# Performance work log

Hardware: AMD Instinct MI355X
Metric: run time of the kernel (lower is better)

The kernel has to match this reference:

```python
import jax, jax.numpy as jnp
import numpy as np

N = 400000
C = 256
H = 512
B = 1024


def setup_inputs() -> dict:
    key = jax.random.key(0)
    k1, k2, k3, k4, k5, k6 = jax.random.split(key, 6)
    x = jax.random.normal(k1, (N, C), dtype=jnp.float32)
    batch = jnp.sort(jax.random.randint(k2, (N,), 0, B, dtype=jnp.int64))
    # Linear params (torch nn.Linear layout: W [out, in], y = x @ W.T + b)
    Wt = jax.random.normal(k3, (H, C), dtype=jnp.float32) / np.sqrt(C)
    bt = jax.random.normal(k4, (H,), dtype=jnp.float32) * 0.01
    Wg = jax.random.normal(k5, (1, H), dtype=jnp.float32) / np.sqrt(H)
    bg = jax.random.normal(k6, (1,), dtype=jnp.float32) * 0.01
    return {"x": x, "batch": batch, "batch_size": B,
            "Wt": Wt, "bt": bt, "Wg": Wg, "bg": bg}


def reference(x, batch, batch_size, Wt, bt, Wg, bg):
    # gate: softplus(Linear(x)) -> Linear -> scalar attention logit per node
    nx = jax.nn.softplus(x @ Wt.T + bt)          # [N, 512]
    logits = (nx @ Wg.T + bg)[:, 0]              # [N]
    # scatter softmax over segments (numerically stable)
    seg_max = jax.ops.segment_max(logits, batch, num_segments=batch_size)
    e = jnp.exp(logits - seg_max[batch])         # [N]
    seg_sum = jax.ops.segment_sum(e, batch, num_segments=batch_size)
    attn = (e / seg_sum[batch])[:, None]         # [N, 1]
    # weighted sum + segment mean
    out_sum = jax.ops.segment_sum(attn * x, batch, num_segments=batch_size)  # [B, C]
    x_sum = jax.ops.segment_sum(x, batch, num_segments=batch_size)
    counts = jax.ops.segment_sum(jnp.ones((x.shape[0],), x.dtype), batch,
                                 num_segments=batch_size)
    mean = x_sum / jnp.maximum(counts, 1.0)[:, None]
    return out_sum + mean
```

## Files before the change

kernel.cpp:

```cpp
#include <hip/hip_runtime.h>
#include <hip/hip_bf16.h>
#include <stdint.h>

typedef __attribute__((ext_vector_type(8))) short short8;
typedef __attribute__((ext_vector_type(16))) float f32x16;

#define CD 256
#define HD 512

static __device__ __forceinline__ unsigned short f2bf(float f) {
    union { float f; unsigned int u; } cv; cv.f = f;
    unsigned int u = cv.u;
    unsigned int r = u + 0x7FFFu + ((u >> 16) & 1u);
    return (unsigned short)(r >> 16);
}
static __device__ __forceinline__ unsigned int pack2(unsigned short a, unsigned short b) {
    return (unsigned int)a | ((unsigned int)b << 16);
}

__global__ void prep_kernel(const float* __restrict__ wt, unsigned short* __restrict__ wtb,
                            const void* __restrict__ batch, int* __restrict__ b32, int n) {
    const int blk = blockIdx.x;
    if (blk < 64) {
        int t = blk * 256 + threadIdx.x;
        const float4* p = (const float4*)wt;
        float4 f0 = p[t * 2], f1 = p[t * 2 + 1];
        uint4 v;
        v.x = pack2(f2bf(f0.x), f2bf(f0.y));
        v.y = pack2(f2bf(f0.z), f2bf(f0.w));
        v.z = pack2(f2bf(f1.x), f2bf(f1.y));
        v.w = pack2(f2bf(f1.z), f2bf(f1.w));
        ((uint4*)wtb)[t] = v;
    } else {
        const long long* p64 = (const long long*)batch;
        const int* p32 = (const int*)batch;
        bool is64 = ((unsigned long long)p64[n / 2 - 1]) < (1ull << 20);
        for (int i = (blk - 64) * 256 + threadIdx.x; i < n; i += 512 * 256)
            b32[i] = is64 ? (int)p64[i] : p32[i];
    }
}

__global__ __launch_bounds__(256) void gate_kernel(
    const float* __restrict__ x, const unsigned short* __restrict__ wtb,
    const float* __restrict__ bt, const float* __restrict__ wg,
    const float* __restrict__ bg, float* __restrict__ logits, int n)
{
    __shared__ __align__(16) char lds[36864];
    const int tid = threadIdx.x;
    const int lane = tid & 63;
    const int wid = tid >> 6;
    const int l31 = lane & 31;
    const int g = lane >> 5;
    const long rowbase = (long)blockIdx.x * 128;

    {
        float2 b2 = ((const float2*)bt)[tid];
        float2 w2 = ((const float2*)wg)[tid];
        *(float2*)(lds + 32768 + tid * 8) = b2;
        *(float2*)(lds + 34816 + tid * 8) = w2;
    }

    short8 a[16];
    {
        const long row = rowbase + wid * 32 + l31;
        const float4* xr = (const float4*)(x + row * 256) + g * 2;
#define CVT_A(kt, F0, F1)                                                             \
        {                                                                             \
            __hip_bfloat162 p0 = __float22bfloat162_rn(make_float2((F0).x, (F0).y));  \
            __hip_bfloat162 p1 = __float22bfloat162_rn(make_float2((F0).z, (F0).w));  \
            __hip_bfloat162 p2 = __float22bfloat162_rn(make_float2((F1).x, (F1).y));  \
            __hip_bfloat162 p3 = __float22bfloat162_rn(make_float2((F1).z, (F1).w));  \
            union { uint4 u; short8 s; } cv;                                          \
            cv.u = make_uint4(*(unsigned int*)&p0, *(unsigned int*)&p1,               \
                              *(unsigned int*)&p2, *(unsigned int*)&p3);              \
            a[kt] = cv.s;                                                             \
        }
        if (rowbase + 128 <= (long)n) {
#pragma unroll
            for (int kt = 0; kt < 16; ++kt) {
                float4 f0 = xr[kt * 4];
                float4 f1 = xr[kt * 4 + 1];
                CVT_A(kt, f0, f1)
            }
        } else {
            const bool ok = row < (long)n;
#pragma unroll
            for (int kt = 0; kt < 16; ++kt) {
                float4 f0 = ok ? xr[kt * 4]     : make_float4(0.f, 0.f, 0.f, 0.f);
                float4 f1 = ok ? xr[kt * 4 + 1] : make_float4(0.f, 0.f, 0.f, 0.f);
                CVT_A(kt, f0, f1)
            }
        }
#undef CVT_A
    }

    int soff[4];
#pragma unroll
    for (int i = 0; i < 4; ++i) {
        int p = (wid * 4 + i) * 64 + lane;
        int rc = p >> 5;
        int gcl = (p & 31) ^ (rc & 31);
        soff[i] = rc * 512 + gcl * 16;
    }
    const char* wtbb = (const char*)wtb;

#define STAGE(c, bufoff)                                                              \
    {                                                                                 \
        const char* src = wtbb + (c) * 16384;                                         \
        char* dst = lds + (bufoff) + wid * 4096;                                      \
        _Pragma("unroll")                                                             \
        for (int i = 0; i < 4; ++i)                                                   \
            __builtin_amdgcn_global_load_lds(                                         \
                (const __attribute__((address_space(1))) unsigned int*)(src + soff[i]), \
                (__attribute__((address_space(3))) unsigned int*)(dst + i * 1024),    \
                16, 0, 0);                                                            \
    }

#define COMPUTE(c)                                                                    \
    {                                                                                 \
        const char* bb = lds + ((c) & 1) * 16384 + l31 * 512;                         \
        f32x16 acc;                                                                   \
        _Pragma("unroll")                                                             \
        for (int r = 0; r < 16; ++r) acc[r] = 0.f;                                    \
        _Pragma("unroll")                                                             \
        for (int kt = 0; kt < 16; ++kt) {                                             \
            short8 b = *(const short8*)(bb + (((kt * 2 + g) ^ l31) * 16));            \
            acc = __builtin_amdgcn_mfma_f32_32x32x16_bf16(a[kt], b, acc, 0, 0, 0);    \
        }                                                                             \
        const float btv = *(const float*)(lds + 32768 + ((c) * 32 + l31) * 4);        \
        const float wgv = *(const float*)(lds + 34816 + ((c) * 32 + l31) * 4);        \
        _Pragma("unroll")                                                             \
        for (int r = 0; r < 16; ++r) {                                                \
            float v = acc[r] + btv;                                                   \
            float sp = fmaxf(v, 0.f) + __logf(1.f + __expf(-__builtin_fabsf(v)));     \
            lp[r] = fmaf(sp, wgv, lp[r]);                                             \
        }                                                                             \
    }

    float lp[16];
#pragma unroll
    for (int r = 0; r < 16; ++r) lp[r] = 0.f;

    __syncthreads();

    STAGE(0, 0);

#pragma unroll 1
    for (int c = 0; c < 16; ++c) {
        asm volatile("s_waitcnt vmcnt(0)" ::: "memory");
        __builtin_amdgcn_s_barrier();
        if (c < 15) STAGE(c + 1, ((c + 1) & 1) * 16384);
        COMPUTE(c);
    }
#undef COMPUTE
#undef STAGE

#pragma unroll
    for (int r = 0; r < 16; ++r) {
        float v = lp[r];
        v += __shfl_xor(v, 1);
        v += __shfl_xor(v, 2);
        v += __shfl_xor(v, 4);
        v += __shfl_xor(v, 8);
        v += __shfl_xor(v, 16);
        lp[r] = v;
    }
    if (l31 == 0) {
        const float bgv = bg[0];
#pragma unroll
        for (int r = 0; r < 16; ++r) {
            long row = rowbase + wid * 32 + 4 * g + (r & 3) + 8 * (r >> 2);
            if (row < (long)n) logits[row] = lp[r] + bgv;
        }
    }
}

static __device__ __forceinline__ int lower_bound(const int* __restrict__ a, int n, int v) {
    int lo = 0, hi = n;
    while (lo < hi) { int mid = (lo + hi) >> 1; if (a[mid] < v) lo = mid + 1; else hi = mid; }
    return lo;
}

__global__ __launch_bounds__(256) void segpool_kernel(const float* __restrict__ x,
    const float* __restrict__ logits, const int* __restrict__ batch,
    float* __restrict__ out, int n)
{
    __shared__ float wsh[1024];
    __shared__ float sh_red[4];
    __shared__ int sh_se[2];
    const int b = blockIdx.x;
    const int tid = threadIdx.x;

    if (tid == 0) {
        sh_se[0] = lower_bound(batch, n, b);
        sh_se[1] = lower_bound(batch, n, b + 1);
    }
    __syncthreads();
    const int start = sh_se[0], end = sh_se[1];
    const int cnt = end - start;

    float m = -3.4e38f;
    for (int i = start + tid; i < end; i += 256) m = fmaxf(m, logits[i]);
#pragma unroll
    for (int mk = 1; mk <= 32; mk <<= 1) m = fmaxf(m, __shfl_xor(m, mk));
    if ((tid & 63) == 0) sh_red[tid >> 6] = m;
    __syncthreads();
    m = fmaxf(fmaxf(sh_red[0], sh_red[1]), fmaxf(sh_red[2], sh_red[3]));
    __syncthreads();

    float s = 0.f;
    for (int i = start + tid; i < end; i += 256) s += __expf(logits[i] - m);
#pragma unroll
    for (int mk = 1; mk <= 32; mk <<= 1) s += __shfl_xor(s, mk);
    if ((tid & 63) == 0) sh_red[tid >> 6] = s;
    __syncthreads();
    s = sh_red[0] + sh_red[1] + sh_red[2] + sh_red[3];

    const float srs = (s > 0.f) ? (1.f / s) : 0.f;
    const float sinv = 1.f / (float)((cnt > 0) ? cnt : 1);

    float acc = 0.f;
    const int c = tid;
    for (int base = 0; base < cnt; base += 1024) {
        const int mm = min(cnt - base, 1024);
        __syncthreads();
        for (int i = c; i < mm; i += 256)
            wsh[i] = __expf(logits[start + base + i] - m) * srs + sinv;
        __syncthreads();
        const float* xp = x + (size_t)(start + base) * CD + c;
        int i = 0;
        for (; i + 8 <= mm; i += 8) {
            float x0 = xp[(size_t)(i+0)*CD], x1 = xp[(size_t)(i+1)*CD];
            float x2 = xp[(size_t)(i+2)*CD], x3 = xp[(size_t)(i+3)*CD];
            float x4 = xp[(size_t)(i+4)*CD], x5 = xp[(size_t)(i+5)*CD];
            float x6 = xp[(size_t)(i+6)*CD], x7 = xp[(size_t)(i+7)*CD];
            acc = fmaf(wsh[i+0],x0,fmaf(wsh[i+1],x1,fmaf(wsh[i+2],x2,fmaf(wsh[i+3],x3,acc))));
            acc = fmaf(wsh[i+4],x4,fmaf(wsh[i+5],x5,fmaf(wsh[i+6],x6,fmaf(wsh[i+7],x7,acc))));
        }
        for (; i < mm; ++i) acc = fmaf(wsh[i], xp[(size_t)i*CD], acc);
    }
    out[(size_t)b * CD + c] = acc;
}

extern "C" void kernel_launch(void* const* d_in, const int* in_sizes, int n_in,
                              void* d_out, int out_size, void* d_ws, size_t ws_size,
                              hipStream_t stream)
{
    const float* x  = (const float*)d_in[0];
    const void*  batch = d_in[1];
    const float* Wt = (const float*)d_in[3];
    const float* bt = (const float*)d_in[4];
    const float* Wg = (const float*)d_in[5];
    const float* bg = (const float*)d_in[6];
    float* out = (float*)d_out;
    const int n = in_sizes[1];
    const int nseg = out_size / CD;

    char* ws = (char*)d_ws;
    size_t off = 0;
    unsigned short* wtb = (unsigned short*)(ws + off); off += (size_t)HD * CD * 2;
    float* logits = (float*)(ws + off); off += (size_t)n * 4;
    int* batch32  = (int*)(ws + off);   off += (size_t)n * 4;

    hipLaunchKernelGGL(prep_kernel, dim3(576), dim3(256), 0, stream, Wt, wtb, batch, batch32, n);
    hipLaunchKernelGGL(gate_kernel, dim3((n + 127) / 128), dim3(256), 0, stream,
                       x, wtb, bt, Wg, bg, logits, n);
    hipLaunchKernelGGL(segpool_kernel, dim3(nseg), dim3(256), 0, stream,
                       x, logits, batch32, out, n);
}
```

Baseline: 279.0 us.

## Overlap MFMA with previous chunk's softplus and compute softplus in log2 domain

The gate loop is software-pipelined with two accumulators. The MFMA chain for chunk c is issued in the same region as the softplus epilogue of chunk c-1, so matrix-core work and VALU transcendental work can overlap instead of running back to back. Softplus is also rewritten as ln2·log2(1+2^w): LOG2E is folded into the bf16 weights and bias, and LN2 into the gate weights, which drops the max/abs/exp/log sequence for raw exp2/log2 builtins. In exchange it uses more accumulator registers and loses the numerically stable form, so very large pre-activations would overflow to inf.

```diff
diff --git a/kernel.cpp b/kernel.cpp
--- a/kernel.cpp
+++ b/kernel.cpp
@@ -17,6 +17,9 @@
 static __device__ __forceinline__ unsigned int pack2(unsigned short a, unsigned short b) {
     return (unsigned int)a | ((unsigned int)b << 16);
 }
+
+#define LOG2E 1.44269504f
+#define LN2   0.69314718f
 
 __global__ void prep_kernel(const float* __restrict__ wt, unsigned short* __restrict__ wtb,
                             const void* __restrict__ batch, int* __restrict__ b32, int n) {
@@ -26,10 +29,10 @@
         const float4* p = (const float4*)wt;
         float4 f0 = p[t * 2], f1 = p[t * 2 + 1];
         uint4 v;
-        v.x = pack2(f2bf(f0.x), f2bf(f0.y));
-        v.y = pack2(f2bf(f0.z), f2bf(f0.w));
-        v.z = pack2(f2bf(f1.x), f2bf(f1.y));
-        v.w = pack2(f2bf(f1.z), f2bf(f1.w));
+        v.x = pack2(f2bf(f0.x * LOG2E), f2bf(f0.y * LOG2E));
+        v.y = pack2(f2bf(f0.z * LOG2E), f2bf(f0.w * LOG2E));
+        v.z = pack2(f2bf(f1.x * LOG2E), f2bf(f1.y * LOG2E));
+        v.w = pack2(f2bf(f1.z * LOG2E), f2bf(f1.w * LOG2E));
         ((uint4*)wtb)[t] = v;
     } else {
         const long long* p64 = (const long long*)batch;
@@ -56,6 +59,8 @@
     {
         float2 b2 = ((const float2*)bt)[tid];
         float2 w2 = ((const float2*)wg)[tid];
+        b2.x *= LOG2E; b2.y *= LOG2E;
+        w2.x *= LN2;   w2.y *= LN2;
         *(float2*)(lds + 32768 + tid * 8) = b2;
         *(float2*)(lds + 34816 + tid * 8) = w2;
     }
@@ -116,28 +121,41 @@
                 16, 0, 0);                                                            \
     }
 
-#define COMPUTE(c)                                                                    \
+#define MFMA_CHUNK(c, ACC)                                                            \
     {                                                                                 \
         const char* bb = lds + ((c) & 1) * 16384 + l31 * 512;                         \
-        f32x16 acc;                                                                   \
         _Pragma("unroll")                                                             \
-        for (int r = 0; r < 16; ++r) acc[r] = 0.f;                                    \
+        for (int r = 0; r < 16; ++r) ACC[r] = 0.f;                                    \
         _Pragma("unroll")                                                             \
         for (int kt = 0; kt < 16; ++kt) {                                             \
             short8 b = *(const short8*)(bb + (((kt * 2 + g) ^ l31) * 16));            \
-            acc = __builtin_amdgcn_mfma_f32_32x32x16_bf16(a[kt], b, acc, 0, 0, 0);    \
+            ACC = __builtin_amdgcn_mfma_f32_32x32x16_bf16(a[kt], b, ACC, 0, 0, 0);    \
         }                                                                             \
+    }
+
+#define SOFTPLUS(c, PACC)                                                             \
+    {                                                                                 \
         const float btv = *(const float*)(lds + 32768 + ((c) * 32 + l31) * 4);        \
         const float wgv = *(const float*)(lds + 34816 + ((c) * 32 + l31) * 4);        \
         _Pragma("unroll")                                                             \
         for (int r = 0; r < 16; ++r) {                                                \
-            float v = acc[r] + btv;                                                   \
-            float sp = fmaxf(v, 0.f) + __logf(1.f + __expf(-__builtin_fabsf(v)));     \
+            float w = PACC[r] + btv;                                                  \
+            float sp = __builtin_amdgcn_logf(1.0f + __builtin_amdgcn_exp2f(w));       \
             lp[r] = fmaf(sp, wgv, lp[r]);                                             \
         }                                                                             \
     }
 
+#define REGION(c, ACC, PACC)                                                          \
+    {                                                                                 \
+        asm volatile("s_waitcnt vmcnt(0)" ::: "memory");                              \
+        __builtin_amdgcn_s_barrier();                                                 \
+        if ((c) < 15) STAGE((c) + 1, (((c) + 1) & 1) * 16384);                        \
+        MFMA_CHUNK(c, ACC)                                                            \
+        SOFTPLUS((c) - 1, PACC)                                                       \
+    }
+
     float lp[16];
+    f32x16 accA, accB;
 #pragma unroll
     for (int r = 0; r < 16; ++r) lp[r] = 0.f;
 
@@ -145,14 +163,26 @@
 
     STAGE(0, 0);
 
+    asm volatile("s_waitcnt vmcnt(0)" ::: "memory");
+    __builtin_amdgcn_s_barrier();
+    STAGE(1, 16384);
+    MFMA_CHUNK(0, accA)
+
 #pragma unroll 1
-    for (int c = 0; c < 16; ++c) {
+    for (int c = 1; c < 15; c += 2) {
+        REGION(c, accB, accA)
+        REGION(c + 1, accA, accB)
+    }
+    {
         asm volatile("s_waitcnt vmcnt(0)" ::: "memory");
         __builtin_amdgcn_s_barrier();
-        if (c < 15) STAGE(c + 1, ((c + 1) & 1) * 16384);
-        COMPUTE(c);
-    }
-#undef COMPUTE
+        MFMA_CHUNK(15, accB)
+        SOFTPLUS(14, accA)
+    }
+    SOFTPLUS(15, accB)
+#undef REGION
+#undef SOFTPLUS
+#undef MFMA_CHUNK
 #undef STAGE
 
 #pragma unroll
```

Measured after the change: 246.7 us. -11.6%, faster.
